# Optimization experiments

Hardware: AMD Instinct MI355X
Metric: run time of the kernel (lower is better)

## Reference

```python
import jax, jax.numpy as jnp
import numpy as np
import math

NHEAD = 8
IOU_THR = 0.2
COS_THR = 0.2


def _build_mask(segments, q):
    # segments: [bz, Lq, 2] (center, length); q: [bz, Lq, d]
    c, l = segments[..., 0], segments[..., 1]
    s, e = c - l / 2, c + l / 2  # ml2se: midpoint-length -> start-end
    inter = jnp.clip(jnp.minimum(e[:, :, None], e[:, None, :])
                     - jnp.maximum(s[:, :, None], s[:, None, :]), 0.0)
    union = l[:, :, None] + l[:, None, :] - inter
    iou = inter / union  # [bz, Lq, Lq]
    qn = q / jnp.maximum(jnp.linalg.norm(q, axis=-1, keepdims=True), 1e-8)
    cos = jnp.einsum('bid,bjd->bij', qn, qn)
    Lq = q.shape[1]
    adj = jnp.broadcast_to(jnp.eye(Lq, dtype=bool), iou.shape)
    adj = jnp.where(iou <= IOU_THR, True, adj)   # adj_matrix[iou<=0.2]=1
    adj = jnp.where(cos <= COS_THR, False, adj)  # adj_matrix[cos<=0.2]=0
    return ~adj  # True = masked


def setup_inputs() -> dict:
    key = jax.random.key(0)
    ks = jax.random.split(key, 8)
    Lq, bz, d = 1024, 8, 512
    bound = 1.0 / math.sqrt(d)
    query = jax.random.normal(ks[0], (Lq, bz, d), jnp.float32)
    segments = jax.random.uniform(ks[1], (bz, Lq, 2), jnp.float32)
    Wq = jax.random.uniform(ks[2], (d, d), jnp.float32, -bound, bound)
    bq = jax.random.uniform(ks[3], (d,), jnp.float32, -bound, bound)
    Wk = jax.random.uniform(ks[4], (d, d), jnp.float32, -bound, bound)
    bk = jax.random.uniform(ks[5], (d,), jnp.float32, -bound, bound)
    Wv = jax.random.uniform(ks[6], (d, d), jnp.float32, -bound, bound)
    bv = jax.random.uniform(ks[7], (d,), jnp.float32, -bound, bound)
    return dict(query=query, segments=segments, Wq=Wq, bq=bq, Wk=Wk, bk=bk,
                Wv=Wv, bv=bv)


def reference(query, segments, Wq, bq, Wk, bk, Wv, bv):
    Lq, bz, d = query.shape
    dh = d // NHEAD
    h = jnp.transpose(query, (1, 0, 2))  # [bz, Lq, d]
    mask = _build_mask(segments, h)      # [bz, Lq, Lq], bool
    Q = (h @ Wq.T + bq).reshape(bz, Lq, NHEAD, dh)
    K = (h @ Wk.T + bk).reshape(bz, Lq, NHEAD, dh)
    V = (h @ Wv.T + bv).reshape(bz, Lq, NHEAD, dh)
    scores = jnp.einsum('bihd,bjhd->bhij', Q, K) / math.sqrt(dh)
    scores = jnp.where(mask[:, None, :, :], -jnp.inf, scores)
    attn = jax.nn.softmax(scores, axis=-1)
    out = jnp.einsum('bhij,bjhd->bihd', attn, V).reshape(bz, Lq, d) + h
    return jnp.transpose(out, (1, 0, 2))  # [Lq, bz, d]
```

## Files before the change

kernel.cpp:

```cpp
#include <hip/hip_runtime.h>
#include <math.h>

#define LQ 1024
#define BZ 8
#define D  512
#define NH 8
#define DH 64
#define IOU_THR 0.2f
#define COS_THR 0.2f
#define NEG (-1e30f)
#define FIXCAP 16384

typedef short bf16x8 __attribute__((ext_vector_type(8)));
typedef float f32x4  __attribute__((ext_vector_type(4)));

#define MFMA16(a, b, cacc) __builtin_amdgcn_mfma_f32_16x16x32_bf16(a, b, cacc, 0, 0, 0)

__device__ inline unsigned short f2bf(float x) {
    union { float f; unsigned int u; } v; v.f = x;
    unsigned int r = v.u + 0x7FFF + ((v.u >> 16) & 1);
    return (unsigned short)(r >> 16);
}

__device__ __forceinline__ void gload_lds16(const void* g, void* l) {
    __builtin_amdgcn_global_load_lds(
        (const __attribute__((address_space(1))) unsigned int*)g,
        (__attribute__((address_space(3))) unsigned int*)l, 16, 0, 0);
}

__global__ __launch_bounds__(256) void prep_kernel(const float* __restrict__ query,
                                                   const float* __restrict__ Wq,
                                                   const float* __restrict__ Wk,
                                                   const float* __restrict__ Wv,
                                                   unsigned short* __restrict__ hi,
                                                   unsigned short* __restrict__ Wb,
                                                   float* __restrict__ rnorm) {
    int blk = blockIdx.x, tid = threadIdx.x;
    if (blk < 2048) {
        int w = tid >> 6, lane = tid & 63;
        int row = blk * 4 + w;
        int b = row >> 10, i = row & 1023;
        const float* src = query + ((size_t)i * BZ + b) * D + lane * 8;
        float4 v0 = *(const float4*)src;
        float4 v1 = *(const float4*)(src + 4);
        uint4 pk;
        pk.x = (unsigned)f2bf(v0.x) | ((unsigned)f2bf(v0.y) << 16);
        pk.y = (unsigned)f2bf(v0.z) | ((unsigned)f2bf(v0.w) << 16);
        pk.z = (unsigned)f2bf(v1.x) | ((unsigned)f2bf(v1.y) << 16);
        pk.w = (unsigned)f2bf(v1.z) | ((unsigned)f2bf(v1.w) << 16);
        *(uint4*)(hi + (size_t)row * D + lane * 8) = pk;
        float ss = v0.x * v0.x + v0.y * v0.y + v0.z * v0.z + v0.w * v0.w
                 + v1.x * v1.x + v1.y * v1.y + v1.z * v1.z + v1.w * v1.w;
        #pragma unroll
        for (int s = 1; s < 64; s <<= 1) ss += __shfl_xor(ss, s);
        if (lane == 0) rnorm[row] = 1.0f / fmaxf(sqrtf(ss), 1e-8f);
    } else {
        int t = (blk - 2048) * 256 + tid;
        int mat = t >> 16;
        int off = (t & 65535) * 4;
        const float* src = (mat == 0) ? Wq : (mat == 1) ? Wk : Wv;
        float4 v = *(const float4*)(src + off);
        uint2 p;
        p.x = (unsigned)f2bf(v.x) | ((unsigned)f2bf(v.y) << 16);
        p.y = (unsigned)f2bf(v.z) | ((unsigned)f2bf(v.w) << 16);
        *(uint2*)(Wb + (size_t)mat * D * D + off) = p;
    }
}

__global__ __launch_bounds__(256) void gemm_kernel(const unsigned short* __restrict__ hi,
                                                   const unsigned short* __restrict__ Wb,
                                                   const float* __restrict__ rnorm,
                                                   const float* __restrict__ segments,
                                                   const float* __restrict__ bq,
                                                   const float* __restrict__ bk,
                                                   const float* __restrict__ bv,
                                                   unsigned char* __restrict__ mask,
                                                   unsigned char* __restrict__ summ,
                                                   int* __restrict__ fix_cnt,
                                                   unsigned int* __restrict__ fix_list,
                                                   unsigned short* __restrict__ Qb,
                                                   unsigned short* __restrict__ Kb,
                                                   unsigned short* __restrict__ Vt) {
    __shared__ __align__(16) char SMEM[49152];
    __shared__ int summ_lds[8][2], summ_t_lds[8][2];

    int blk = blockIdx.x, tid = threadIdx.x, w = tid >> 6, lane = tid & 63;
    int c = lane & 15, q4 = lane >> 4;
    int wr = w >> 1, wc = w & 1;

    bool is_qkv = blk >= 288;
    const char *Asrc, *Bsrc;
    int b = 0, i0 = 0, j0 = 0, z = 0, m0 = 0, n0 = 0;
    if (is_qkv) {
        int x = blk - 288;
        int g = (x & 7) + 8 * ((x >> 3) / 12);
        int inner = (x >> 3) % 12;
        z = inner >> 2;
        m0 = g * 128;
        n0 = (inner & 3) * 128;
        Asrc = (const char*)(hi + (size_t)m0 * D);
        Bsrc = (const char*)(Wb + (size_t)z * D * D + (size_t)n0 * D);
    } else {
        int x = blk;
        b = x & 7;
        int t = x >> 3;
        int it = 0;
        while (t >= 8 - it) { t -= 8 - it; it++; }
        int jt = it + t;
        i0 = it * 128; j0 = jt * 128;
        Asrc = (const char*)(hi + ((size_t)b * LQ + i0) * D);
        Bsrc = (const char*)(hi + ((size_t)b * LQ + j0) * D);
        if (tid < 16) {
            summ_lds[tid >> 1][tid & 1] = 0;
            summ_t_lds[tid >> 1][tid & 1] = 0;
        }
    }

    int lrow = lane >> 2;
    int gl   = (lane & 3) ^ ((lane >> 3) & 3);
    size_t goff = (size_t)lrow * 1024 + (size_t)gl * 16;

    char* const Ab[3] = { SMEM, SMEM + 8192, SMEM + 16384 };
    char* const Bb[3] = { SMEM + 24576, SMEM + 32768, SMEM + 40960 };

    #pragma unroll
    for (int m = 0; m < 2; m++) {
        int n = 2 * w + m;
        gload_lds16(Asrc + (size_t)n * 16384 + goff, Ab[0] + n * 1024);
        gload_lds16(Bsrc + (size_t)n * 16384 + goff, Bb[0] + n * 1024);
    }
    #pragma unroll
    for (int m = 0; m < 2; m++) {
        int n = 2 * w + m;
        gload_lds16(Asrc + 64 + (size_t)n * 16384 + goff, Ab[1] + n * 1024);
        gload_lds16(Bsrc + 64 + (size_t)n * 16384 + goff, Bb[1] + n * 1024);
    }
    asm volatile("s_waitcnt vmcnt(4)" ::: "memory");
    __builtin_amdgcn_s_barrier();

    f32x4 acc[4][4] = {};
    int rswz = (c >> 1) & 3;
    #pragma unroll
    for (int k = 0; k < 16; k++) {
        char* Ac = Ab[k % 3];
        char* Bc = Bb[k % 3];
        if (k < 14) {
            size_t kb = (size_t)(k + 2) * 64;
            char* An = Ab[(k + 2) % 3];
            char* Bn = Bb[(k + 2) % 3];
            #pragma unroll
            for (int m = 0; m < 2; m++) {
                int n = 2 * w + m;
                gload_lds16(Asrc + kb + (size_t)n * 16384 + goff, An + n * 1024);
                gload_lds16(Bsrc + kb + (size_t)n * 16384 + goff, Bn + n * 1024);
            }
        }
        bf16x8 af[4], bf[4];
        #pragma unroll
        for (int f = 0; f < 4; f++) {
            af[f] = *(const bf16x8*)(Ac + ((wr * 64 + f * 16 + c) * 32 + (q4 ^ rswz) * 8) * 2);
            bf[f] = *(const bf16x8*)(Bc + ((wc * 64 + f * 16 + c) * 32 + (q4 ^ rswz) * 8) * 2);
        }
        asm volatile("s_waitcnt lgkmcnt(0)" ::: "memory");
        __builtin_amdgcn_sched_barrier(0);
        __builtin_amdgcn_s_setprio(1);
        #pragma unroll
        for (int fr = 0; fr < 4; fr++)
            #pragma unroll
            for (int fc = 0; fc < 4; fc++)
                acc[fr][fc] = MFMA16(af[fr], bf[fc], acc[fr][fc]);
        __builtin_amdgcn_s_setprio(0);
        if (k < 15) {
            if (k < 14) asm volatile("s_waitcnt vmcnt(4)" ::: "memory");
            else        asm volatile("s_waitcnt vmcnt(0)" ::: "memory");
            __builtin_amdgcn_s_barrier();
        }
    }
    __builtin_amdgcn_s_barrier();

    if (is_qkv) {
        const float* bias = (z == 0) ? bq : (z == 1) ? bk : bv;
        #pragma unroll
        for (int fr = 0; fr < 4; fr++)
            #pragma unroll
            for (int r = 0; r < 4; r++) {
                int row = wr * 64 + fr * 16 + q4 * 4 + r;
                char* rbase = SMEM + row * 272 + (row >> 3) * 16;
                #pragma unroll
                for (int fc = 0; fc < 4; fc++) {
                    int col = wc * 64 + fc * 16 + c;
                    *(unsigned short*)(rbase + col * 2) =
                        f2bf(acc[fr][fc][r] + bias[n0 + col]);
                }
            }
        __syncthreads();
        int bb = m0 >> 10, ib = m0 & 1023;
        if (z < 2) {
            unsigned short* dst = (z == 0) ? Qb : Kb;
            #pragma unroll
            for (int it2 = 0; it2 < 8; it2++) {
                int idx = it2 * 256 + tid;
                int row = idx >> 4, cg = idx & 15;
                uint4 v = *(const uint4*)(SMEM + row * 272 + (row >> 3) * 16 + cg * 16);
                int n = n0 + cg * 8;
                int hh = n >> 6, dh = n & 63;
                *(uint4*)(dst + (((size_t)bb * NH + hh) * LQ + ib + row) * DH + dh) = v;
            }
        } else {
            #pragma unroll
            for (int it2 = 0; it2 < 8; it2++) {
                int idx = it2 * 256 + tid;
                int rowg = idx & 15, colI = idx >> 4;
                union { unsigned short s[8]; uint4 v; } u;
                char* gbase = SMEM + rowg * 16;
                #pragma unroll
                for (int rr = 0; rr < 8; rr++)
                    u.s[rr] = *(const unsigned short*)(gbase + (rowg * 8 + rr) * 272 + colI * 2);
                int n = n0 + colI;
                int hh = n >> 6, dh = n & 63;
                *(uint4*)(Vt + (((size_t)bb * NH + hh) * DH + dh) * LQ + ib + rowg * 8) = u.v;
            }
        }
    } else {
        float4* iSE = (float4*)SMEM;
        float4* jSE = (float4*)(SMEM + 2048);
        const float2* seg2 = (const float2*)(segments + (size_t)b * LQ * 2);
        const float* rn = rnorm + b * LQ;
        if (tid < 128) {
            float2 cl = seg2[i0 + tid];
            iSE[tid] = make_float4(cl.x - cl.y * 0.5f, cl.x + cl.y * 0.5f, cl.y, rn[i0 + tid]);
        } else {
            float2 cl = seg2[j0 + tid - 128];
            jSE[tid - 128] = make_float4(cl.x - cl.y * 0.5f, cl.x + cl.y * 0.5f, cl.y, rn[j0 + tid - 128]);
        }
        __syncthreads();

        bool offdiag = (i0 != j0);
        unsigned char* mbase = mask + ((size_t)b << 20);
        int anyT[4] = {0, 0, 0, 0};
        #pragma unroll
        for (int fr = 0; fr < 4; fr++) {
            int anyun = 0;
            unsigned int tpack[4] = {0, 0, 0, 0};
            #pragma unroll
            for (int r = 0; r < 4; r++) {
                int il = wr * 64 + fr * 16 + q4 * 4 + r;
                int i = i0 + il;
                float4 I = iSE[il];
                #pragma unroll
                for (int fc = 0; fc < 4; fc++) {
                    int jl = wc * 64 + fc * 16 + c;
                    int j = j0 + jl;
                    float4 J = jSE[jl];
                    float cosv = acc[fr][fc][r] * I.w * J.w;
                    if (fabsf(cosv - COS_THR) < 1.5e-3f) {
                        int idx = atomicAdd(fix_cnt, 1);
                        if (idx < FIXCAP)
                            fix_list[idx] = ((unsigned int)b << 20) | ((unsigned int)i << 10) | j;
                    }
                    float inter = fmaxf(fminf(I.y, J.y) - fmaxf(I.x, J.x), 0.0f);
                    float uni   = I.z + J.z - inter;
                    float iou   = inter / uni;
                    bool adj = ((iou <= IOU_THR) || (i == j)) && (cosv > COS_THR);
                    mbase[(size_t)i * LQ + j] = adj ? 0 : 1;
                    tpack[fc] |= (adj ? 0u : 1u) << (8 * r);
                    anyun |= adj ? 1 : 0;
                    anyT[fc] |= adj ? 1 : 0;
                }
            }
            if (anyun) atomicOr(&summ_lds[wr * 4 + fr][wc], 1);
            if (offdiag) {
                int ibase = i0 + wr * 64 + fr * 16 + q4 * 4;
                #pragma unroll
                for (int fc = 0; fc < 4; fc++) {
                    int j = j0 + wc * 64 + fc * 16 + c;
                    *(unsigned int*)&mbase[(size_t)j * LQ + ibase] = tpack[fc];
                }
            }
        }
        if (offdiag) {
            #pragma unroll
            for (int fc = 0; fc < 4; fc++)
                if (anyT[fc]) atomicOr(&summ_t_lds[wc * 4 + fc][wr], 1);
        }
        __syncthreads();
        if (tid < 16) {
            int lit = tid >> 1, ljt = tid & 1;
            summ[((size_t)b * 64 + (i0 >> 4) + lit) * 16 + (j0 >> 6) + ljt] =
                summ_lds[lit][ljt] ? 1 : 0;
            if (offdiag)
                summ[((size_t)b * 64 + (j0 >> 4) + lit) * 16 + (i0 >> 6) + ljt] =
                    summ_t_lds[lit][ljt] ? 1 : 0;
        }
    }
}

__global__ __launch_bounds__(64) void fixup_kernel(const float* __restrict__ query,
                                                   const float* __restrict__ rnorm,
                                                   const float* __restrict__ segments,
                                                   const int* __restrict__ fix_cnt,
                                                   const unsigned int* __restrict__ fix_list,
                                                   unsigned char* __restrict__ mask,
                                                   unsigned char* __restrict__ summ) {
    int cnt = *fix_cnt; if (cnt > FIXCAP) cnt = FIXCAP;
    int lane = threadIdx.x;
    for (int e = blockIdx.x; e < cnt; e += gridDim.x) {
        unsigned int pk = fix_list[e];
        int b = pk >> 20, i = (pk >> 10) & 1023, j = pk & 1023;
        const float* hri = query + ((size_t)i * BZ + b) * D;
        const float* hrj = query + ((size_t)j * BZ + b) * D;
        double dd = 0.0;
        #pragma unroll
        for (int k = 0; k < D / 64; k++)
            dd += (double)hri[k * 64 + lane] * (double)hrj[k * 64 + lane];
        #pragma unroll
        for (int s = 1; s < 64; s <<= 1) dd += __shfl_xor(dd, s);
        if (lane == 0) {
            float rni = rnorm[b * LQ + i], rnj = rnorm[b * LQ + j];
            float cosv = (float)(dd * (double)rni * (double)rnj);
            const float* seg = segments + (size_t)b * LQ * 2;
            float ci = seg[i * 2], li = seg[i * 2 + 1];
            float cj = seg[j * 2], lj = seg[j * 2 + 1];
            float si = ci - li * 0.5f, ei = ci + li * 0.5f;
            float sj = cj - lj * 0.5f, ej = cj + lj * 0.5f;
            float inter = fmaxf(fminf(ei, ej) - fmaxf(si, sj), 0.0f);
            float iou = inter / (li + lj - inter);
            bool adj = ((iou <= IOU_THR) || (i == j)) && (cosv > COS_THR);
            unsigned char mv = adj ? 0 : 1;
            mask[((size_t)b * LQ + i) * LQ + j] = mv;
            mask[((size_t)b * LQ + j) * LQ + i] = mv;
            if (adj) {
                summ[((size_t)b * 64 + (i >> 4)) * 16 + (j >> 6)] = 1;
                summ[((size_t)b * 64 + (j >> 4)) * 16 + (i >> 6)] = 1;
            }
        }
    }
}

__global__ __launch_bounds__(256) void attn_kernel(const unsigned short* __restrict__ Qb,
                                                   const unsigned short* __restrict__ Kb,
                                                   const unsigned short* __restrict__ Vt,
                                                   const unsigned char* __restrict__ mask,
                                                   const unsigned char* __restrict__ summ,
                                                   const float* __restrict__ query,
                                                   float* __restrict__ out) {
    int tid = threadIdx.x;
    int w = tid >> 6, lane = tid & 63;
    int c = lane & 15, q4 = lane >> 4;
    int hh = blockIdx.y, b = blockIdx.z;
    int i0 = blockIdx.x * 64 + w * 16;
    size_t bh = (size_t)b * NH + hh;

    __shared__ unsigned short p_lds[4][16][72];

    const unsigned short* Qrow = Qb + (bh * LQ + i0 + c) * DH;
    bf16x8 qa0 = *(const bf16x8*)(Qrow + q4 * 8);
    bf16x8 qa1 = *(const bf16x8*)(Qrow + 32 + q4 * 8);

    f32x4 O[4] = {};
    float m_r[4] = {NEG, NEG, NEG, NEG};
    float l_r[4] = {0.f, 0.f, 0.f, 0.f};

    const unsigned short* Kbase = Kb + bh * LQ * DH;
    const unsigned short* Vbase = Vt + bh * DH * LQ;
    const unsigned char*  mbase = mask + ((size_t)b * LQ + i0) * LQ;
    const unsigned char*  srow  = summ + ((size_t)b * 64 + (i0 >> 4)) * 16;

    for (int jt = 0; jt < 16; jt++) {
        if (!srow[jt]) continue;
        int j0 = jt * 64;
        f32x4 S[4] = {};
        #pragma unroll
        for (int cb = 0; cb < 4; cb++) {
            const unsigned short* krow = Kbase + (size_t)(j0 + cb * 16 + c) * DH;
            bf16x8 kf0 = *(const bf16x8*)(krow + q4 * 8);
            bf16x8 kf1 = *(const bf16x8*)(krow + 32 + q4 * 8);
            S[cb] = MFMA16(qa0, kf0, S[cb]);
            S[cb] = MFMA16(qa1, kf1, S[cb]);
        }
        float p[4][4];
        float tmax[4] = {NEG, NEG, NEG, NEG};
        #pragma unroll
        for (int cb = 0; cb < 4; cb++)
            #pragma unroll
            for (int r = 0; r < 4; r++) {
                float sc = S[cb][r] * 0.125f;
                unsigned char mm = mbase[(size_t)(q4 * 4 + r) * LQ + j0 + cb * 16 + c];
                sc = mm ? NEG : sc;
                p[cb][r] = sc;
                tmax[r] = fmaxf(tmax[r], sc);
            }
        #pragma unroll
        for (int r = 0; r < 4; r++) {
            float v = tmax[r];
            v = fmaxf(v, __shfl_xor(v, 1));
            v = fmaxf(v, __shfl_xor(v, 2));
            v = fmaxf(v, __shfl_xor(v, 4));
            v = fmaxf(v, __shfl_xor(v, 8));
            tmax[r] = v;
        }
        float rsum[4];
        #pragma unroll
        for (int r = 0; r < 4; r++) {
            float mn = fmaxf(m_r[r], tmax[r]);
            float alpha = __expf(m_r[r] - mn);
            m_r[r] = mn;
            l_r[r] *= alpha;
            #pragma unroll
            for (int cb2 = 0; cb2 < 4; cb2++) O[cb2][r] *= alpha;
            float s0 = 0.f;
            #pragma unroll
            for (int cb = 0; cb < 4; cb++) {
                float e = __expf(p[cb][r] - mn);
                p[cb][r] = e;
                s0 += e;
            }
            rsum[r] = s0;
        }
        #pragma unroll
        for (int r = 0; r < 4; r++) {
            float v = rsum[r];
            v += __shfl_xor(v, 1);
            v += __shfl_xor(v, 2);
            v += __shfl_xor(v, 4);
            v += __shfl_xor(v, 8);
            l_r[r] += v;
        }
        #pragma unroll
        for (int cb = 0; cb < 4; cb++)
            #pragma unroll
            for (int r = 0; r < 4; r++)
                p_lds[w][q4 * 4 + r][cb * 16 + c] = f2bf(p[cb][r]);
        #pragma unroll
        for (int s = 0; s < 2; s++) {
            bf16x8 pf = *(const bf16x8*)&p_lds[w][c][s * 32 + q4 * 8];
            #pragma unroll
            for (int cb = 0; cb < 4; cb++) {
                bf16x8 vf = *(const bf16x8*)(Vbase + (size_t)(cb * 16 + c) * LQ + j0 + s * 32 + q4 * 8);
                O[cb] = MFMA16(pf, vf, O[cb]);
            }
        }
    }
    #pragma unroll
    for (int r = 0; r < 4; r++) {
        int i = i0 + q4 * 4 + r;
        float inv = 1.0f / l_r[r];
        #pragma unroll
        for (int cb = 0; cb < 4; cb++) {
            int col = hh * 64 + cb * 16 + c;
            size_t oidx = ((size_t)i * BZ + b) * D + col;
            out[oidx] = O[cb][r] * inv + query[oidx];
        }
    }
}

extern "C" void kernel_launch(void* const* d_in, const int* in_sizes, int n_in,
                              void* d_out, int out_size, void* d_ws, size_t ws_size,
                              hipStream_t stream) {
    const float* query    = (const float*)d_in[0];
    const float* segments = (const float*)d_in[1];
    const float* Wq = (const float*)d_in[2];
    const float* bq = (const float*)d_in[3];
    const float* Wk = (const float*)d_in[4];
    const float* bk = (const float*)d_in[5];
    const float* Wv = (const float*)d_in[6];
    const float* bv = (const float*)d_in[7];
    float* out = (float*)d_out;

    const size_t NTOK = (size_t)BZ * LQ;
    char* ws = (char*)d_ws;
    unsigned short* hbuf  = (unsigned short*)ws;   ws += NTOK * D * 2;
    unsigned short* Qb    = (unsigned short*)ws;   ws += NTOK * D * 2;
    unsigned short* Kb    = (unsigned short*)ws;   ws += NTOK * D * 2;
    unsigned short* Vt    = (unsigned short*)ws;   ws += NTOK * D * 2;
    unsigned short* Wb    = (unsigned short*)ws;   ws += (size_t)3 * D * D * 2;
    float*          rnorm = (float*)ws;            ws += NTOK * 4;
    unsigned char*  mask  = (unsigned char*)ws;    ws += (size_t)BZ * LQ * LQ;
    unsigned char*  summ  = (unsigned char*)ws;    ws += 8192;
    int*            fix_cnt = (int*)ws;            ws += 64;
    unsigned int*   fix_list = (unsigned int*)ws;

    hipMemsetAsync(fix_cnt, 0, 64, stream);
    prep_kernel<<<2816, 256, 0, stream>>>(query, Wq, Wk, Wv, hbuf, Wb, rnorm);
    gemm_kernel<<<1056, 256, 0, stream>>>(hbuf, Wb, rnorm, segments, bq, bk, bv,
                                          mask, summ, fix_cnt, fix_list, Qb, Kb, Vt);
    fixup_kernel<<<64, 64, 0, stream>>>(query, rnorm, segments, fix_cnt, fix_list, mask, summ);
    attn_kernel<<<dim3(LQ / 64, NH, BZ), 256, 0, stream>>>(Qb, Kb, Vt, mask, summ, query, out);
}
```

Baseline: 142.7 us.

## Enlarge gemm tiles to 256x128 and fold fix_cnt reset into prep kernel

The fused mask/QKV GEMM kernel now computes 256x128 output tiles per block instead of 128x128. Each wave holds 8x4 MFMA accumulators, LDS grows to 72KB, and the grid shrinks from 1056 to 544 blocks. The Gram-matrix tile enumeration is reworked so that every tile writes its transposed mask half, including diagonal-straddling tiles. The separate memset of the fixup counter is replaced by a store inside prep_kernel, removing one launch. Larger tiles cut redundant operand loads but raise register pressure and lower occupancy, and they leave fewer blocks to spread across CUs.

```diff
diff --git a/kernel.cpp b/kernel.cpp
--- a/kernel.cpp
+++ b/kernel.cpp
@@ -34,7 +34,8 @@
                                                    const float* __restrict__ Wv,
                                                    unsigned short* __restrict__ hi,
                                                    unsigned short* __restrict__ Wb,
-                                                   float* __restrict__ rnorm) {
+                                                   float* __restrict__ rnorm,
+                                                   int* __restrict__ fix_cnt) {
     int blk = blockIdx.x, tid = threadIdx.x;
     if (blk < 2048) {
         int w = tid >> 6, lane = tid & 63;
@@ -55,6 +56,7 @@
         for (int s = 1; s < 64; s <<= 1) ss += __shfl_xor(ss, s);
         if (lane == 0) rnorm[row] = 1.0f / fmaxf(sqrtf(ss), 1e-8f);
     } else {
+        if (blk == 2048 && tid == 0) *fix_cnt = 0;
         int t = (blk - 2048) * 256 + tid;
         int mat = t >> 16;
         int off = (t & 65535) * 4;
@@ -67,52 +69,53 @@
     }
 }
 
-__global__ __launch_bounds__(256) void gemm_kernel(const unsigned short* __restrict__ hi,
-                                                   const unsigned short* __restrict__ Wb,
-                                                   const float* __restrict__ rnorm,
-                                                   const float* __restrict__ segments,
-                                                   const float* __restrict__ bq,
-                                                   const float* __restrict__ bk,
-                                                   const float* __restrict__ bv,
-                                                   unsigned char* __restrict__ mask,
-                                                   unsigned char* __restrict__ summ,
-                                                   int* __restrict__ fix_cnt,
-                                                   unsigned int* __restrict__ fix_list,
-                                                   unsigned short* __restrict__ Qb,
-                                                   unsigned short* __restrict__ Kb,
-                                                   unsigned short* __restrict__ Vt) {
-    __shared__ __align__(16) char SMEM[49152];
-    __shared__ int summ_lds[8][2], summ_t_lds[8][2];
+__global__ __launch_bounds__(256, 2) void gemm_kernel(const unsigned short* __restrict__ hi,
+                                                      const unsigned short* __restrict__ Wb,
+                                                      const float* __restrict__ rnorm,
+                                                      const float* __restrict__ segments,
+                                                      const float* __restrict__ bq,
+                                                      const float* __restrict__ bk,
+                                                      const float* __restrict__ bv,
+                                                      unsigned char* __restrict__ mask,
+                                                      unsigned char* __restrict__ summ,
+                                                      int* __restrict__ fix_cnt,
+                                                      unsigned int* __restrict__ fix_list,
+                                                      unsigned short* __restrict__ Qb,
+                                                      unsigned short* __restrict__ Kb,
+                                                      unsigned short* __restrict__ Vt) {
+    __shared__ __align__(16) char SMEM[73728];
+    __shared__ int summ_d[16][2], summ_t[8][4];
 
     int blk = blockIdx.x, tid = threadIdx.x, w = tid >> 6, lane = tid & 63;
     int c = lane & 15, q4 = lane >> 4;
-    int wr = w >> 1, wc = w & 1;
-
-    bool is_qkv = blk >= 288;
+    int wr2 = w >> 1, wc2 = w & 1;
+
+    bool is_qkv = blk >= 160;
     const char *Asrc, *Bsrc;
     int b = 0, i0 = 0, j0 = 0, z = 0, m0 = 0, n0 = 0;
     if (is_qkv) {
-        int x = blk - 288;
+        int x = blk - 160;
         int g = (x & 7) + 8 * ((x >> 3) / 12);
         int inner = (x >> 3) % 12;
         z = inner >> 2;
-        m0 = g * 128;
+        m0 = g * 256;
         n0 = (inner & 3) * 128;
         Asrc = (const char*)(hi + (size_t)m0 * D);
         Bsrc = (const char*)(Wb + (size_t)z * D * D + (size_t)n0 * D);
     } else {
-        int x = blk;
-        b = x & 7;
-        int t = x >> 3;
-        int it = 0;
-        while (t >= 8 - it) { t -= 8 - it; it++; }
-        int jt = it + t;
-        i0 = it * 128; j0 = jt * 128;
+        b = blk & 7;
+        int t = blk >> 3;
+        int it, jt;
+        if (t < 8)       { it = 0; jt = t; }
+        else if (t < 14) { it = 1; jt = 2 + (t - 8); }
+        else if (t < 18) { it = 2; jt = 4 + (t - 14); }
+        else             { it = 3; jt = 6 + (t - 18); }
+        i0 = it * 256; j0 = jt * 128;
         Asrc = (const char*)(hi + ((size_t)b * LQ + i0) * D);
         Bsrc = (const char*)(hi + ((size_t)b * LQ + j0) * D);
-        if (tid < 16) {
-            summ_lds[tid >> 1][tid & 1] = 0;
-            summ_t_lds[tid >> 1][tid & 1] = 0;
+        if (tid < 32) {
+            summ_d[tid >> 1][tid & 1] = 0;
+            summ_t[tid >> 2][tid & 3] = 0;
         }
     }
 
@@ -120,136 +123,136 @@
     int gl   = (lane & 3) ^ ((lane >> 3) & 3);
     size_t goff = (size_t)lrow * 1024 + (size_t)gl * 16;
 
-    char* const Ab[3] = { SMEM, SMEM + 8192, SMEM + 16384 };
-    char* const Bb[3] = { SMEM + 24576, SMEM + 32768, SMEM + 40960 };
-
-    #pragma unroll
-    for (int m = 0; m < 2; m++) {
-        int n = 2 * w + m;
-        gload_lds16(Asrc + (size_t)n * 16384 + goff, Ab[0] + n * 1024);
-        gload_lds16(Bsrc + (size_t)n * 16384 + goff, Bb[0] + n * 1024);
-    }
-    #pragma unroll
-    for (int m = 0; m < 2; m++) {
-        int n = 2 * w + m;
-        gload_lds16(Asrc + 64 + (size_t)n * 16384 + goff, Ab[1] + n * 1024);
-        gload_lds16(Bsrc + 64 + (size_t)n * 16384 + goff, Bb[1] + n * 1024);
-    }
-    asm volatile("s_waitcnt vmcnt(4)" ::: "memory");
+    char* const Abuf[3] = { SMEM, SMEM + 16384, SMEM + 32768 };
+    char* const Bbuf[3] = { SMEM + 49152, SMEM + 57344, SMEM + 65536 };
+
+#define STAGE_STEP(kb, Ad, Bd) do {                                            \
+    _Pragma("unroll")                                                          \
+    for (int m_ = 0; m_ < 4; m_++)                                             \
+        gload_lds16(Asrc + (kb) + (size_t)(4 * w + m_) * 16384 + goff,         \
+                    (Ad) + (4 * w + m_) * 1024);                               \
+    _Pragma("unroll")                                                          \
+    for (int m_ = 0; m_ < 2; m_++)                                             \
+        gload_lds16(Bsrc + (kb) + (size_t)(2 * w + m_) * 16384 + goff,         \
+                    (Bd) + (2 * w + m_) * 1024);                               \
+} while (0)
+
+    STAGE_STEP((size_t)0, Abuf[0], Bbuf[0]);
+    STAGE_STEP((size_t)64, Abuf[1], Bbuf[1]);
+    asm volatile("s_waitcnt vmcnt(6)" ::: "memory");
     __builtin_amdgcn_s_barrier();
 
-    f32x4 acc[4][4] = {};
+    f32x4 acc[8][4] = {};
     int rswz = (c >> 1) & 3;
     #pragma unroll
     for (int k = 0; k < 16; k++) {
-        char* Ac = Ab[k % 3];
-        char* Bc = Bb[k % 3];
-        if (k < 14) {
-            size_t kb = (size_t)(k + 2) * 64;
-            char* An = Ab[(k + 2) % 3];
-            char* Bn = Bb[(k + 2) % 3];
-            #pragma unroll
-            for (int m = 0; m < 2; m++) {
-                int n = 2 * w + m;
-                gload_lds16(Asrc + kb + (size_t)n * 16384 + goff, An + n * 1024);
-                gload_lds16(Bsrc + kb + (size_t)n * 16384 + goff, Bn + n * 1024);
-            }
-        }
-        bf16x8 af[4], bf[4];
-        #pragma unroll
-        for (int f = 0; f < 4; f++) {
-            af[f] = *(const bf16x8*)(Ac + ((wr * 64 + f * 16 + c) * 32 + (q4 ^ rswz) * 8) * 2);
-            bf[f] = *(const bf16x8*)(Bc + ((wc * 64 + f * 16 + c) * 32 + (q4 ^ rswz) * 8) * 2);
-        }
+        char* Ac = Abuf[k % 3];
+        char* Bc = Bbuf[k % 3];
+        if (k < 14)
+            STAGE_STEP((size_t)(k + 2) * 64, Abuf[(k + 2) % 3], Bbuf[(k + 2) % 3]);
+        bf16x8 af[8], bf[4];
+        #pragma unroll
+        for (int f = 0; f < 8; f++)
+            af[f] = *(const bf16x8*)(Ac + ((wr2 * 128 + f * 16 + c) * 32 + (q4 ^ rswz) * 8) * 2);
+        #pragma unroll
+        for (int f = 0; f < 4; f++)
+            bf[f] = *(const bf16x8*)(Bc + ((wc2 * 64 + f * 16 + c) * 32 + (q4 ^ rswz) * 8) * 2);
         asm volatile("s_waitcnt lgkmcnt(0)" ::: "memory");
         __builtin_amdgcn_sched_barrier(0);
         __builtin_amdgcn_s_setprio(1);
         #pragma unroll
-        for (int fr = 0; fr < 4; fr++)
+        for (int fr = 0; fr < 8; fr++)
             #pragma unroll
             for (int fc = 0; fc < 4; fc++)
                 acc[fr][fc] = MFMA16(af[fr], bf[fc], acc[fr][fc]);
         __builtin_amdgcn_s_setprio(0);
         if (k < 15) {
-            if (k < 14) asm volatile("s_waitcnt vmcnt(4)" ::: "memory");
+            if (k < 14) asm volatile("s_waitcnt vmcnt(6)" ::: "memory");
             else        asm volatile("s_waitcnt vmcnt(0)" ::: "memory");
             __builtin_amdgcn_s_barrier();
         }
     }
+#undef STAGE_STEP
     __builtin_amdgcn_s_barrier();
 
     if (is_qkv) {
         const float* bias = (z == 0) ? bq : (z == 1) ? bk : bv;
         #pragma unroll
-        for (int fr = 0; fr < 4; fr++)
-            #pragma unroll
-            for (int r = 0; r < 4; r++) {
-                int row = wr * 64 + fr * 16 + q4 * 4 + r;
-                char* rbase = SMEM + row * 272 + (row >> 3) * 16;
+        for (int h = 0; h < 2; h++) {
+            if (wr2 == h) {
                 #pragma unroll
-                for (int fc = 0; fc < 4; fc++) {
-                    int col = wc * 64 + fc * 16 + c;
-                    *(unsigned short*)(rbase + col * 2) =
-                        f2bf(acc[fr][fc][r] + bias[n0 + col]);
+                for (int fr = 0; fr < 8; fr++)
+                    #pragma unroll
+                    for (int r = 0; r < 4; r++) {
+                        int row = fr * 16 + q4 * 4 + r;
+                        char* rbase = SMEM + row * 272 + (row >> 3) * 16;
+                        #pragma unroll
+                        for (int fc = 0; fc < 4; fc++) {
+                            int col = wc2 * 64 + fc * 16 + c;
+                            *(unsigned short*)(rbase + col * 2) =
+                                f2bf(acc[fr][fc][r] + bias[n0 + col]);
+                        }
+                    }
+            }
+            __syncthreads();
+            int rbase0 = m0 + h * 128;
+            int bb = rbase0 >> 10, ib = rbase0 & 1023;
+            if (z < 2) {
+                unsigned short* dst = (z == 0) ? Qb : Kb;
+                #pragma unroll
+                for (int it2 = 0; it2 < 8; it2++) {
+                    int idx = it2 * 256 + tid;
+                    int row = idx >> 4, cg = idx & 15;
+                    uint4 v = *(const uint4*)(SMEM + row * 272 + (row >> 3) * 16 + cg * 16);
+                    int n = n0 + cg * 8;
+                    int hh = n >> 6, dh = n & 63;
+                    *(uint4*)(dst + (((size_t)bb * NH + hh) * LQ + ib + row) * DH + dh) = v;
                 }
-            }
-        __syncthreads();
-        int bb = m0 >> 10, ib = m0 & 1023;
-        if (z < 2) {
-            unsigned short* dst = (z == 0) ? Qb : Kb;
-            #pragma unroll
-            for (int it2 = 0; it2 < 8; it2++) {
-                int idx = it2 * 256 + tid;
-                int row = idx >> 4, cg = idx & 15;
-                uint4 v = *(const uint4*)(SMEM + row * 272 + (row >> 3) * 16 + cg * 16);
-                int n = n0 + cg * 8;
-                int hh = n >> 6, dh = n & 63;
-                *(uint4*)(dst + (((size_t)bb * NH + hh) * LQ + ib + row) * DH + dh) = v;
-            }
-        } else {
-            #pragma unroll
-            for (int it2 = 0; it2 < 8; it2++) {
-                int idx = it2 * 256 + tid;
-                int rowg = idx & 15, colI = idx >> 4;
-                union { unsigned short s[8]; uint4 v; } u;
-                char* gbase = SMEM + rowg * 16;
+            } else {
                 #pragma unroll
-                for (int rr = 0; rr < 8; rr++)
-                    u.s[rr] = *(const unsigned short*)(gbase + (rowg * 8 + rr) * 272 + colI * 2);
-                int n = n0 + colI;
-                int hh = n >> 6, dh = n & 63;
-                *(uint4*)(Vt + (((size_t)bb * NH + hh) * DH + dh) * LQ + ib + rowg * 8) = u.v;
-            }
+                for (int it2 = 0; it2 < 8; it2++) {
+                    int idx = it2 * 256 + tid;
+                    int rowg = idx & 15, colI = idx >> 4;
+                    union { unsigned short s[8]; uint4 v; } u;
+                    char* gbase = SMEM + rowg * 16;
+                    #pragma unroll
+                    for (int rr = 0; rr < 8; rr++)
+                        u.s[rr] = *(const unsigned short*)(gbase + (rowg * 8 + rr) * 272 + colI * 2);
+                    int n = n0 + colI;
+                    int hh = n >> 6, dh = n & 63;
+                    *(uint4*)(Vt + (((size_t)bb * NH + hh) * DH + dh) * LQ + ib + rowg * 8) = u.v;
+                }
+            }
+            __syncthreads();
         }
     } else {
         float4* iSE = (float4*)SMEM;
-        float4* jSE = (float4*)(SMEM + 2048);
+        float4* jSE = (float4*)(SMEM + 4096);
         const float2* seg2 = (const float2*)(segments + (size_t)b * LQ * 2);
         const float* rn = rnorm + b * LQ;
-        if (tid < 128) {
+        {
             float2 cl = seg2[i0 + tid];
             iSE[tid] = make_float4(cl.x - cl.y * 0.5f, cl.x + cl.y * 0.5f, cl.y, rn[i0 + tid]);
-        } else {
-            float2 cl = seg2[j0 + tid - 128];
-            jSE[tid - 128] = make_float4(cl.x - cl.y * 0.5f, cl.x + cl.y * 0.5f, cl.y, rn[j0 + tid - 128]);
+            if (tid < 128) {
+                float2 cl2 = seg2[j0 + tid];
+                jSE[tid] = make_float4(cl2.x - cl2.y * 0.5f, cl2.x + cl2.y * 0.5f, cl2.y, rn[j0 + tid]);
+            }
         }
         __syncthreads();
 
-        bool offdiag = (i0 != j0);
         unsigned char* mbase = mask + ((size_t)b << 20);
-        int anyT[4] = {0, 0, 0, 0};
-        #pragma unroll
-        for (int fr = 0; fr < 4; fr++) {
+        #pragma unroll
+        for (int fr = 0; fr < 8; fr++) {
             int anyun = 0;
             unsigned int tpack[4] = {0, 0, 0, 0};
             #pragma unroll
             for (int r = 0; r < 4; r++) {
-                int il = wr * 64 + fr * 16 + q4 * 4 + r;
+                int il = wr2 * 128 + fr * 16 + q4 * 4 + r;
                 int i = i0 + il;
                 float4 I = iSE[il];
                 #pragma unroll
                 for (int fc = 0; fc < 4; fc++) {
-                    int jl = wc * 64 + fc * 16 + c;
+                    int jl = wc2 * 64 + fc * 16 + c;
                     int j = j0 + jl;
                     float4 J = jSE[jl];
                     float cosv = acc[fr][fc][r] * I.w * J.w;
@@ -265,32 +268,28 @@
                     mbase[(size_t)i * LQ + j] = adj ? 0 : 1;
                     tpack[fc] |= (adj ? 0u : 1u) << (8 * r);
                     anyun |= adj ? 1 : 0;
-                    anyT[fc] |= adj ? 1 : 0;
                 }
             }
-            if (anyun) atomicOr(&summ_lds[wr * 4 + fr][wc], 1);
-            if (offdiag) {
-                int ibase = i0 + wr * 64 + fr * 16 + q4 * 4;
-                #pragma unroll
-                for (int fc = 0; fc < 4; fc++) {
-                    int j = j0 + wc * 64 + fc * 16 + c;
-                    *(unsigned int*)&mbase[(size_t)j * LQ + ibase] = tpack[fc];
-                }
-            }
-        }
-        if (offdiag) {
-            #pragma unroll
-            for (int fc = 0; fc < 4; fc++)
-                if (anyT[fc]) atomicOr(&summ_t_lds[wc * 4 + fc][wr], 1);
+            if (anyun) atomicOr(&summ_d[wr2 * 8 + fr][wc2], 1);
+            int ibase = i0 + wr2 * 128 + fr * 16 + q4 * 4;
+            #pragma unroll
+            for (int fc = 0; fc < 4; fc++) {
+                int j = j0 + wc2 * 64 + fc * 16 + c;
+                *(unsigned int*)&mbase[(size_t)j * LQ + ibase] = tpack[fc];
+                if (tpack[fc] != 0x01010101u)
+                    atomicOr(&summ_t[wc2 * 4 + fc][wr2 * 2 + (fr >> 2)], 1);
+            }
         }
         __syncthreads();
-        if (tid < 16) {
-            int lit = tid >> 1, ljt = tid & 1;
-            summ[((size_t)b * 64 + (i0 >> 4) + lit) * 16 + (j0 >> 6) + ljt] =
-                summ_lds[lit][ljt] ? 1 : 0;
-            if (offdiag)
-                summ[((size_t)b * 64 + (j0 >> 4) + lit) * 16 + (i0 >> 6) + ljt] =
-                    summ_t_lds[lit][ljt] ? 1 : 0;
+        if (tid < 32) {
+            int r = tid >> 1, cc = tid & 1;
+            summ[((size_t)b * 64 + (i0 >> 4) + r) * 16 + (j0 >> 6) + cc] =
+                summ_d[r][cc] ? 1 : 0;
+        } else if (tid < 64) {
+            int t2 = tid - 32;
+            int r = t2 >> 2, cc = t2 & 3;
+            summ[((size_t)b * 64 + (j0 >> 4) + r) * 16 + (i0 >> 6) + cc] =
+                summ_t[r][cc] ? 1 : 0;
         }
     }
 }
@@ -480,10 +479,9 @@
     int*            fix_cnt = (int*)ws;            ws += 64;
     unsigned int*   fix_list = (unsigned int*)ws;
 
-    hipMemsetAsync(fix_cnt, 0, 64, stream);
-    prep_kernel<<<2816, 256, 0, stream>>>(query, Wq, Wk, Wv, hbuf, Wb, rnorm);
-    gemm_kernel<<<1056, 256, 0, stream>>>(hbuf, Wb, rnorm, segments, bq, bk, bv,
-                                          mask, summ, fix_cnt, fix_list, Qb, Kb, Vt);
+    prep_kernel<<<2816, 256, 0, stream>>>(query, Wq, Wk, Wv, hbuf, Wb, rnorm, fix_cnt);
+    gemm_kernel<<<544, 256, 0, stream>>>(hbuf, Wb, rnorm, segments, bq, bk, bv,
+                                         mask, summ, fix_cnt, fix_list, Qb, Kb, Vt);
     fixup_kernel<<<64, 64, 0, stream>>>(query, rnorm, segments, fix_cnt, fix_list, mask, summ);
     attn_kernel<<<dim3(LQ / 64, NH, BZ), 256, 0, stream>>>(Qb, Kb, Vt, mask, summ, query, out);
 }
```

Result: slower. 187.1 us (+31.1%).
